# Kernel optimization log

Hardware: AMD Instinct MI355X
Metric: run time of the kernel (lower is better)

## Reference

```python
import jax, jax.numpy as jnp
import numpy as np

N_DYADIC = 0   # dyadic refinement order (init kwarg n)
SOLVER = 0     # first-order explicit finite-difference scheme (init kwarg solver)


def _solve_goursat(inc):
    """Solve Goursat PDE K_{p+1,q+1} = K_{p+1,q} + K_{p,q+1} - K_{p,q} + inc[p,q]*K_{p,q}
    with boundary K[0,:] = K[:,0] = 1. inc: [B, P, Q] -> returns K[P,Q] per pair: [B]."""
    B, P, Q = inc.shape
    dt = inc.dtype
    ones_b = jnp.ones((B,), dt)

    def row_step(prev_row, inc_row):
        # prev_row: [B, Q+1] = K[p, :]; inc_row: [B, Q]
        def col_step(k_left, t):
            k_diag, k_up, a = t  # K[p,q], K[p,q+1], inc[p,q], each [B]
            k_new = k_up + (k_left - k_diag) + a * k_diag
            return k_new, k_new
        xs = (prev_row[:, :-1].T, prev_row[:, 1:].T, inc_row.T)  # [Q, B] each
        _, tail = jax.lax.scan(col_step, ones_b, xs)              # tail: [Q, B]
        new_row = jnp.concatenate([ones_b[:, None], tail.T], axis=1)
        return new_row, None

    final_row, _ = jax.lax.scan(row_step, jnp.ones((B, Q + 1), dt), jnp.swapaxes(inc, 0, 1))
    return final_row[:, -1]


def _sig_kernel_gram(X, Y, n=N_DYADIC):
    """Signature-kernel Gram matrix. X: [A, M, D], Y: [B, N, D] -> [A, B]."""
    dX = X[:, 1:, :] - X[:, :-1, :]          # [A, M-1, D]
    dY = Y[:, 1:, :] - Y[:, :-1, :]          # [B, N-1, D]
    Minc = jnp.einsum('apd,bqd->abpq', dX, dY)  # pairwise increment inner products
    f = 2 ** n
    if f > 1:  # dyadic grid refinement: split each cell into f*f subcells
        Minc = jnp.repeat(jnp.repeat(Minc, f, axis=2), f, axis=3) / (f * f)
    A, B, P, Q = Minc.shape
    K = _solve_goursat(Minc.reshape(A * B, P, Q))
    return K.reshape(A, B)


def setup_inputs() -> dict:
    key = jax.random.key(0)
    kx, ky = jax.random.split(key)
    SCALE = 0.05  # small Brownian-like increments keep the exponential kernel tame
    X = jnp.cumsum(SCALE * jax.random.normal(kx, (64, 128, 64), dtype=jnp.float32), axis=1)
    Y = jnp.cumsum(SCALE * jax.random.normal(ky, (64, 128, 64), dtype=jnp.float32), axis=1)
    return {"X": X, "Y": Y}


def reference(X, Y):
    K_XX = _sig_kernel_gram(X, X)
    K_YY = _sig_kernel_gram(Y, Y)
    K_XY = _sig_kernel_gram(X, Y)
    dist = jnp.mean(K_XX) + jnp.mean(K_YY) - 2.0 * jnp.mean(K_XY)
    return jnp.mean((X[:, 0, :] - Y[:, 0, :]) ** 2) + dist
```

## Files before the change

### kernel.cpp

```cpp
#include <hip/hip_runtime.h>
#include <math.h>

#define DD 64
#define MM 128
#define RS 133
#define OD 66

typedef float  f32x4v __attribute__((ext_vector_type(4)));
typedef __bf16 bf16x8 __attribute__((ext_vector_type(8)));

#define FOR8(F) F(0) F(1) F(2) F(3) F(4) F(5) F(6) F(7)

union FragU { unsigned int u[4]; bf16x8 v; };

__device__ __forceinline__ unsigned cvtpk(float lo, float hi) {
    unsigned r;
    asm("v_cvt_pk_bf16_f32 %0, %1, %2" : "=v"(r) : "v"(lo), "v"(hi));
    return r;
}

__device__ __forceinline__ bf16x8 dfrag_hi(const float* __restrict__ r0,
                                           const float* __restrict__ r1) {
    float4 a0 = *(const float4*)r0, a1 = *(const float4*)(r0 + 4);
    float4 b0 = *(const float4*)r1, b1 = *(const float4*)(r1 + 4);
    FragU f;
    f.u[0] = cvtpk(b0.x - a0.x, b0.y - a0.y);
    f.u[1] = cvtpk(b0.z - a0.z, b0.w - a0.w);
    f.u[2] = cvtpk(b1.x - a1.x, b1.y - a1.y);
    f.u[3] = cvtpk(b1.z - a1.z, b1.w - a1.w);
    return f.v;
}

__device__ __forceinline__ void dfrag_hilo(const float* __restrict__ r0,
                                           const float* __restrict__ r1,
                                           bf16x8& hi, bf16x8& lo) {
    float4 a0 = *(const float4*)r0, a1 = *(const float4*)(r0 + 4);
    float4 b0 = *(const float4*)r1, b1 = *(const float4*)(r1 + 4);
    float d0 = b0.x - a0.x, d1 = b0.y - a0.y, d2 = b0.z - a0.z, d3 = b0.w - a0.w;
    float d4 = b1.x - a1.x, d5 = b1.y - a1.y, d6 = b1.z - a1.z, d7 = b1.w - a1.w;
    FragU H, L;
    H.u[0] = cvtpk(d0, d1); H.u[1] = cvtpk(d2, d3);
    H.u[2] = cvtpk(d4, d5); H.u[3] = cvtpk(d6, d7);
    float e0 = d0 - __uint_as_float(H.u[0] << 16);
    float e1 = d1 - __uint_as_float(H.u[0] & 0xffff0000u);
    float e2 = d2 - __uint_as_float(H.u[1] << 16);
    float e3 = d3 - __uint_as_float(H.u[1] & 0xffff0000u);
    float e4 = d4 - __uint_as_float(H.u[2] << 16);
    float e5 = d5 - __uint_as_float(H.u[2] & 0xffff0000u);
    float e6 = d6 - __uint_as_float(H.u[3] << 16);
    float e7 = d7 - __uint_as_float(H.u[3] & 0xffff0000u);
    L.u[0] = cvtpk(e0, e1); L.u[1] = cvtpk(e2, e3);
    L.u[2] = cvtpk(e4, e5); L.u[3] = cvtpk(e6, e7);
    hi = H.v; lo = L.v;
}

template<int CTRL, int RM, bool BC>
__device__ __forceinline__ float dpp_add(float x) {
    int t = __builtin_amdgcn_update_dpp(0, __float_as_int(x), CTRL, RM, 0xf, BC);
    return x + __int_as_float(t);
}
__device__ __forceinline__ float wave_incl_scan(float x) {
    x = dpp_add<0x111, 0xf, true >(x);
    x = dpp_add<0x112, 0xf, true >(x);
    x = dpp_add<0x114, 0xf, true >(x);
    x = dpp_add<0x118, 0xf, true >(x);
    x = dpp_add<0x142, 0xa, false>(x);
    x = dpp_add<0x143, 0xc, false>(x);
    return x;
}

__global__ __launch_bounds__(64, 3) void sig_goursat_kernel(
        const float* __restrict__ X, const float* __restrict__ Y,
        float* __restrict__ Kout)
{
    const int bid = blockIdx.x;
    int g, a, b;
    if (bid < 4160) {
        g = bid < 2080 ? 0 : 1;
        const int t = bid - g * 2080;
        float sq = sqrtf(4160.25f - 2.0f * (float)t);
        a = (int)(64.5f - sq);
        if (a < 0) a = 0; if (a > 63) a = 63;
        while (a > 0  && (a * (129 - a)) / 2 > t) --a;
        while (a < 63 && ((a + 1) * (128 - a)) / 2 <= t) ++a;
        b = a + (t - (a * (129 - a)) / 2);
    } else {
        const int t = bid - 4160;
        g = 2; a = t >> 6; b = t & 63;
    }

    const float* __restrict__ U = (g == 1 ? Y : X) + (size_t)a * (MM * DD);
    const float* __restrict__ V = (g == 0 ? X : Y) + (size_t)b * (MM * DD);

    const int lane = threadIdx.x;
    const int l15  = lane & 15;
    const int k8   = (lane >> 4) * 8;
    const int rowg = (lane >> 4) * 4;

    __shared__ float incL[16 * RS];

#define TBDECL(ct) bf16x8 tb0_##ct, tb1_##ct;
    FOR8(TBDECL)
#define TBUILD(ct) { int brow_ = ct * 16 + l15; if (brow_ > 126) brow_ = 126; \
        const float* vp_ = V + (size_t)brow_ * DD + k8; \
        tb0_##ct = dfrag_hi(vp_,      vp_ + DD); \
        tb1_##ct = dfrag_hi(vp_ + 32, vp_ + DD + 32); }
    FOR8(TBUILD)

    float KL0 = 1.0f, KL1 = 1.0f;
    const int wbase = rowg * RS + ((l15 & 1) ? OD : 0) + (l15 >> 1);

#define CTSTEP(ct) { f32x4v acc = {0.f, 0.f, 0.f, 0.f}; \
        acc = __builtin_amdgcn_mfma_f32_16x16x32_bf16(ahi0, tb0_##ct, acc, 0, 0, 0); \
        acc = __builtin_amdgcn_mfma_f32_16x16x32_bf16(alo0, tb0_##ct, acc, 0, 0, 0); \
        acc = __builtin_amdgcn_mfma_f32_16x16x32_bf16(ahi1, tb1_##ct, acc, 0, 0, 0); \
        acc = __builtin_amdgcn_mfma_f32_16x16x32_bf16(alo1, tb1_##ct, acc, 0, 0, 0); \
        const int w_ = wbase + ct * 8; \
        incL[w_]          = acc[0]; \
        incL[w_ + RS]     = acc[1]; \
        incL[w_ + 2*RS]   = acc[2]; \
        incL[w_ + 3*RS]   = acc[3]; }

#define SCANROW(r) { \
        const float iE = incL[(r) * RS + lane]; \
        const float iO = incL[(r) * RS + OD + lane]; \
        const float m0 = iE * KL0; \
        const float m1 = iO * KL1; \
        const float t_ = m0 + m1; \
        const float S_ = wave_incl_scan(t_); \
        const float ex = S_ - t_; \
        KL1 += ex + m0; \
        KL0 += ex; }

    for (int band = 0; band < 8; ++band) {
        int arow = band * 16 + l15; if (arow > 126) arow = 126;
        const float* ap = U + (size_t)arow * DD + k8;
        bf16x8 ahi0, alo0, ahi1, alo1;
        dfrag_hilo(ap,      ap + DD,      ahi0, alo0);
        dfrag_hilo(ap + 32, ap + DD + 32, ahi1, alo1);

        FOR8(CTSTEP)

        #pragma unroll
        for (int r = 0; r < 15; ++r) { SCANROW(r) }
        if (band < 7) { SCANROW(15) }
    }

    if (lane == 63) Kout[(size_t)g * 4096 + a * 64 + b] = KL1;
}

__global__ void sig_reduce_kernel(const float* __restrict__ X,
                                  const float* __restrict__ Y,
                                  const float* __restrict__ Kws,
                                  float* __restrict__ out)
{
    const int t = threadIdx.x;
    double accK = 0.0, acc2 = 0.0;
    for (int i = t; i < 4096; i += 256) {
        const int a = i >> 6, b = i & 63;
        if (a <= b) {
            const double w = (a == b) ? 1.0 : 2.0;
            accK += w * (double)Kws[i];
            accK += w * (double)Kws[4096 + i];
        }
        accK -= 2.0 * (double)Kws[8192 + i];
        const float df = X[(size_t)a * (MM * DD) + b] - Y[(size_t)a * (MM * DD) + b];
        acc2 += (double)df * (double)df;
    }
    __shared__ double red[256];
    red[t] = accK / 4096.0 + acc2 / 4096.0;
    __syncthreads();
    for (int s = 128; s > 0; s >>= 1) {
        if (t < s) red[t] += red[t + s];
        __syncthreads();
    }
    if (t == 0) out[0] = (float)red[0];
}

extern "C" void kernel_launch(void* const* d_in, const int* in_sizes, int n_in,
                              void* d_out, int out_size, void* d_ws, size_t ws_size,
                              hipStream_t stream) {
    const float* X = (const float*)d_in[0];
    const float* Y = (const float*)d_in[1];
    float* Kws = (float*)d_ws;
    float* out = (float*)d_out;

    sig_goursat_kernel<<<dim3(8256), dim3(64), 0, stream>>>(X, Y, Kws);
    sig_reduce_kernel<<<dim3(1), dim3(256), 0, stream>>>(X, Y, Kws, out);
}
```

Measured before the change: 140.1 us.

## Process two Goursat pairs per wave and drop bf16 lo-split for A operand

Each block now handles two row-paths against the same column path, so the V-side bf16 fragments are built once and reused for both. The two independent wave scans are interleaved, so each hides the other's DPP latency, and the grid size is halved. The A-operand hi/lo bf16 split is also dropped, which halves the MFMA count but lowers the precision of the increment inner products. Occupancy bound drops from 3 to 2 waves, and LDS use doubles.

```diff
diff --git a/kernel.cpp b/kernel.cpp
--- a/kernel.cpp
+++ b/kernel.cpp
@@ -5,6 +5,7 @@
 #define MM 128
 #define RS 133
 #define OD 66
+#define P1 2128
 
 typedef float  f32x4v __attribute__((ext_vector_type(4)));
 typedef __bf16 bf16x8 __attribute__((ext_vector_type(8)));
@@ -31,29 +32,6 @@
     return f.v;
 }
 
-__device__ __forceinline__ void dfrag_hilo(const float* __restrict__ r0,
-                                           const float* __restrict__ r1,
-                                           bf16x8& hi, bf16x8& lo) {
-    float4 a0 = *(const float4*)r0, a1 = *(const float4*)(r0 + 4);
-    float4 b0 = *(const float4*)r1, b1 = *(const float4*)(r1 + 4);
-    float d0 = b0.x - a0.x, d1 = b0.y - a0.y, d2 = b0.z - a0.z, d3 = b0.w - a0.w;
-    float d4 = b1.x - a1.x, d5 = b1.y - a1.y, d6 = b1.z - a1.z, d7 = b1.w - a1.w;
-    FragU H, L;
-    H.u[0] = cvtpk(d0, d1); H.u[1] = cvtpk(d2, d3);
-    H.u[2] = cvtpk(d4, d5); H.u[3] = cvtpk(d6, d7);
-    float e0 = d0 - __uint_as_float(H.u[0] << 16);
-    float e1 = d1 - __uint_as_float(H.u[0] & 0xffff0000u);
-    float e2 = d2 - __uint_as_float(H.u[1] << 16);
-    float e3 = d3 - __uint_as_float(H.u[1] & 0xffff0000u);
-    float e4 = d4 - __uint_as_float(H.u[2] << 16);
-    float e5 = d5 - __uint_as_float(H.u[2] & 0xffff0000u);
-    float e6 = d6 - __uint_as_float(H.u[3] << 16);
-    float e7 = d7 - __uint_as_float(H.u[3] & 0xffff0000u);
-    L.u[0] = cvtpk(e0, e1); L.u[1] = cvtpk(e2, e3);
-    L.u[2] = cvtpk(e4, e5); L.u[3] = cvtpk(e6, e7);
-    hi = H.v; lo = L.v;
-}
-
 template<int CTRL, int RM, bool BC>
 __device__ __forceinline__ float dpp_add(float x) {
     int t = __builtin_amdgcn_update_dpp(0, __float_as_int(x), CTRL, RM, 0xf, BC);
@@ -69,35 +47,40 @@
     return x;
 }
 
-__global__ __launch_bounds__(64, 3) void sig_goursat_kernel(
+__global__ __launch_bounds__(64, 2) void sig_goursat_kernel(
         const float* __restrict__ X, const float* __restrict__ Y,
         float* __restrict__ Kout)
 {
     const int bid = blockIdx.x;
-    int g, a, b;
-    if (bid < 4160) {
-        g = bid < 2080 ? 0 : 1;
-        const int t = bid - g * 2080;
-        float sq = sqrtf(4160.25f - 2.0f * (float)t);
-        a = (int)(64.5f - sq);
-        if (a < 0) a = 0; if (a > 63) a = 63;
-        while (a > 0  && (a * (129 - a)) / 2 > t) --a;
-        while (a < 63 && ((a + 1) * (128 - a)) / 2 <= t) ++a;
-        b = a + (t - (a * (129 - a)) / 2);
+    int g, a0, a1, bcol;
+    bool dup = false;
+    if (bid < 2112) {
+        g = bid < 1056 ? 0 : 1;
+        const int t = bid - g * 1056;
+        bcol = (int)(2.0f * sqrtf((float)t + 1.0f));
+        if (bcol > 63) bcol = 63;
+        while (bcol > 0  && ((bcol + 1) * (bcol + 1)) / 4 > t) --bcol;
+        while (bcol < 63 && ((bcol + 2) * (bcol + 2)) / 4 <= t) ++bcol;
+        const int j = t - ((bcol + 1) * (bcol + 1)) / 4;
+        a0 = 2 * j; a1 = 2 * j + 1;
+        if (a1 > bcol) { a1 = a0; dup = true; }
     } else {
-        const int t = bid - 4160;
-        g = 2; a = t >> 6; b = t & 63;
+        const int t = bid - 2112;
+        g = 2; bcol = t & 63;
+        a0 = (t >> 6) * 2; a1 = a0 + 1;
     }
 
-    const float* __restrict__ U = (g == 1 ? Y : X) + (size_t)a * (MM * DD);
-    const float* __restrict__ V = (g == 0 ? X : Y) + (size_t)b * (MM * DD);
+    const float* __restrict__ Ub = (g == 1 ? Y : X);
+    const float* __restrict__ U0 = Ub + (size_t)a0 * (MM * DD);
+    const float* __restrict__ U1 = Ub + (size_t)a1 * (MM * DD);
+    const float* __restrict__ V  = (g == 0 ? X : Y) + (size_t)bcol * (MM * DD);
 
     const int lane = threadIdx.x;
     const int l15  = lane & 15;
     const int k8   = (lane >> 4) * 8;
     const int rowg = (lane >> 4) * 4;
 
-    __shared__ float incL[16 * RS];
+    __shared__ float incL[2 * P1];
 
 #define TBDECL(ct) bf16x8 tb0_##ct, tb1_##ct;
     FOR8(TBDECL)
@@ -107,46 +90,65 @@
         tb1_##ct = dfrag_hi(vp_ + 32, vp_ + DD + 32); }
     FOR8(TBUILD)
 
-    float KL0 = 1.0f, KL1 = 1.0f;
+    float s0e = 1.0f, s0o = 1.0f;
+    float s1e = 1.0f, s1o = 1.0f;
     const int wbase = rowg * RS + ((l15 & 1) ? OD : 0) + (l15 >> 1);
 
-#define CTSTEP(ct) { f32x4v acc = {0.f, 0.f, 0.f, 0.f}; \
-        acc = __builtin_amdgcn_mfma_f32_16x16x32_bf16(ahi0, tb0_##ct, acc, 0, 0, 0); \
-        acc = __builtin_amdgcn_mfma_f32_16x16x32_bf16(alo0, tb0_##ct, acc, 0, 0, 0); \
-        acc = __builtin_amdgcn_mfma_f32_16x16x32_bf16(ahi1, tb1_##ct, acc, 0, 0, 0); \
-        acc = __builtin_amdgcn_mfma_f32_16x16x32_bf16(alo1, tb1_##ct, acc, 0, 0, 0); \
+#define CTSTEP2(ct) { \
+        f32x4v c0 = {0.f, 0.f, 0.f, 0.f}, c1 = {0.f, 0.f, 0.f, 0.f}; \
+        c0 = __builtin_amdgcn_mfma_f32_16x16x32_bf16(a0k0, tb0_##ct, c0, 0, 0, 0); \
+        c1 = __builtin_amdgcn_mfma_f32_16x16x32_bf16(a1k0, tb0_##ct, c1, 0, 0, 0); \
+        c0 = __builtin_amdgcn_mfma_f32_16x16x32_bf16(a0k1, tb1_##ct, c0, 0, 0, 0); \
+        c1 = __builtin_amdgcn_mfma_f32_16x16x32_bf16(a1k1, tb1_##ct, c1, 0, 0, 0); \
         const int w_ = wbase + ct * 8; \
-        incL[w_]          = acc[0]; \
-        incL[w_ + RS]     = acc[1]; \
-        incL[w_ + 2*RS]   = acc[2]; \
-        incL[w_ + 3*RS]   = acc[3]; }
+        incL[w_]             = c0[0]; \
+        incL[w_ + RS]        = c0[1]; \
+        incL[w_ + 2*RS]      = c0[2]; \
+        incL[w_ + 3*RS]      = c0[3]; \
+        incL[P1 + w_]        = c1[0]; \
+        incL[P1 + w_ + RS]   = c1[1]; \
+        incL[P1 + w_ + 2*RS] = c1[2]; \
+        incL[P1 + w_ + 3*RS] = c1[3]; }
 
-#define SCANROW(r) { \
-        const float iE = incL[(r) * RS + lane]; \
-        const float iO = incL[(r) * RS + OD + lane]; \
-        const float m0 = iE * KL0; \
-        const float m1 = iO * KL1; \
-        const float t_ = m0 + m1; \
-        const float S_ = wave_incl_scan(t_); \
-        const float ex = S_ - t_; \
-        KL1 += ex + m0; \
-        KL0 += ex; }
+#define SCANROW2(r) { \
+        const float iE0 = incL[(r) * RS + lane]; \
+        const float iO0 = incL[(r) * RS + OD + lane]; \
+        const float iE1 = incL[P1 + (r) * RS + lane]; \
+        const float iO1 = incL[P1 + (r) * RS + OD + lane]; \
+        const float m0a = iE0 * s0e; \
+        const float m1a = iO0 * s0o; \
+        const float m0b = iE1 * s1e; \
+        const float m1b = iO1 * s1o; \
+        const float ta  = m0a + m1a; \
+        const float tb  = m0b + m1b; \
+        const float Sa  = wave_incl_scan(ta); \
+        const float Sb  = wave_incl_scan(tb); \
+        const float exa = Sa - ta; \
+        const float exb = Sb - tb; \
+        s0o += exa + m0a;  s0e += exa; \
+        s1o += exb + m0b;  s1e += exb; }
 
     for (int band = 0; band < 8; ++band) {
         int arow = band * 16 + l15; if (arow > 126) arow = 126;
-        const float* ap = U + (size_t)arow * DD + k8;
-        bf16x8 ahi0, alo0, ahi1, alo1;
-        dfrag_hilo(ap,      ap + DD,      ahi0, alo0);
-        dfrag_hilo(ap + 32, ap + DD + 32, ahi1, alo1);
+        const float* ap0 = U0 + (size_t)arow * DD + k8;
+        const float* ap1 = U1 + (size_t)arow * DD + k8;
+        bf16x8 a0k0 = dfrag_hi(ap0,      ap0 + DD);
+        bf16x8 a0k1 = dfrag_hi(ap0 + 32, ap0 + DD + 32);
+        bf16x8 a1k0 = dfrag_hi(ap1,      ap1 + DD);
+        bf16x8 a1k1 = dfrag_hi(ap1 + 32, ap1 + DD + 32);
 
-        FOR8(CTSTEP)
+        FOR8(CTSTEP2)
 
         #pragma unroll
-        for (int r = 0; r < 15; ++r) { SCANROW(r) }
-        if (band < 7) { SCANROW(15) }
+        for (int r = 0; r < 15; ++r) { SCANROW2(r) }
+        if (band < 7) { SCANROW2(15) }
     }
 
-    if (lane == 63) Kout[(size_t)g * 4096 + a * 64 + b] = KL1;
+    if (lane == 63) {
+        float* kg = Kout + (size_t)g * 4096;
+        kg[a0 * 64 + bcol] = s0o;
+        if (!dup) kg[a1 * 64 + bcol] = s1o;
+    }
 }
 
 __global__ void sig_reduce_kernel(const float* __restrict__ X,
@@ -185,6 +187,6 @@
     float* Kws = (float*)d_ws;
     float* out = (float*)d_out;
 
-    sig_goursat_kernel<<<dim3(8256), dim3(64), 0, stream>>>(X, Y, Kws);
+    sig_goursat_kernel<<<dim3(4160), dim3(64), 0, stream>>>(X, Y, Kws);
     sig_reduce_kernel<<<dim3(1), dim3(256), 0, stream>>>(X, Y, Kws, out);
 }
```

New measurement: 125.4 us. -10.5%, faster.

## Split MFMA producer and scan consumer into separate waves with double buffering

Applied to the files above, without the earlier changes.

The kernel now uses two waves per block. One wave computes increment-matrix bands with MFMA into a double-buffered shared tile, and the other runs the wavefront scan on the previous band, with a __syncthreads per band. It also drops the bf16 hi/lo split-precision correction, halving MFMA work at some accuracy cost, and changes the LDS layout so the scan reads float2 pairs with prefetch. The aim is to overlap matrix compute with the serial scan. The producer/consumer barrier count must match exactly, and the accuracy loss from dropping the lo terms may matter.

```diff
diff --git a/kernel.cpp b/kernel.cpp
--- a/kernel.cpp
+++ b/kernel.cpp
@@ -3,8 +3,8 @@
 
 #define DD 64
 #define MM 128
-#define RS 133
-#define OD 66
+#define RSW 132
+#define BUFW 2112
 
 typedef float  f32x4v __attribute__((ext_vector_type(4)));
 typedef __bf16 bf16x8 __attribute__((ext_vector_type(8)));
@@ -31,29 +31,6 @@
     return f.v;
 }
 
-__device__ __forceinline__ void dfrag_hilo(const float* __restrict__ r0,
-                                           const float* __restrict__ r1,
-                                           bf16x8& hi, bf16x8& lo) {
-    float4 a0 = *(const float4*)r0, a1 = *(const float4*)(r0 + 4);
-    float4 b0 = *(const float4*)r1, b1 = *(const float4*)(r1 + 4);
-    float d0 = b0.x - a0.x, d1 = b0.y - a0.y, d2 = b0.z - a0.z, d3 = b0.w - a0.w;
-    float d4 = b1.x - a1.x, d5 = b1.y - a1.y, d6 = b1.z - a1.z, d7 = b1.w - a1.w;
-    FragU H, L;
-    H.u[0] = cvtpk(d0, d1); H.u[1] = cvtpk(d2, d3);
-    H.u[2] = cvtpk(d4, d5); H.u[3] = cvtpk(d6, d7);
-    float e0 = d0 - __uint_as_float(H.u[0] << 16);
-    float e1 = d1 - __uint_as_float(H.u[0] & 0xffff0000u);
-    float e2 = d2 - __uint_as_float(H.u[1] << 16);
-    float e3 = d3 - __uint_as_float(H.u[1] & 0xffff0000u);
-    float e4 = d4 - __uint_as_float(H.u[2] << 16);
-    float e5 = d5 - __uint_as_float(H.u[2] & 0xffff0000u);
-    float e6 = d6 - __uint_as_float(H.u[3] << 16);
-    float e7 = d7 - __uint_as_float(H.u[3] & 0xffff0000u);
-    L.u[0] = cvtpk(e0, e1); L.u[1] = cvtpk(e2, e3);
-    L.u[2] = cvtpk(e4, e5); L.u[3] = cvtpk(e6, e7);
-    hi = H.v; lo = L.v;
-}
-
 template<int CTRL, int RM, bool BC>
 __device__ __forceinline__ float dpp_add(float x) {
     int t = __builtin_amdgcn_update_dpp(0, __float_as_int(x), CTRL, RM, 0xf, BC);
@@ -69,7 +46,7 @@
     return x;
 }
 
-__global__ __launch_bounds__(64, 3) void sig_goursat_kernel(
+__global__ __launch_bounds__(128, 4) void sig_goursat_kernel(
         const float* __restrict__ X, const float* __restrict__ Y,
         float* __restrict__ Kout)
 {
@@ -89,64 +66,89 @@
         g = 2; a = t >> 6; b = t & 63;
     }
 
-    const float* __restrict__ U = (g == 1 ? Y : X) + (size_t)a * (MM * DD);
-    const float* __restrict__ V = (g == 0 ? X : Y) + (size_t)b * (MM * DD);
+    const int tid  = threadIdx.x;
+    const int wid  = tid >> 6;
+    const int lane = tid & 63;
 
-    const int lane = threadIdx.x;
-    const int l15  = lane & 15;
-    const int k8   = (lane >> 4) * 8;
-    const int rowg = (lane >> 4) * 4;
+    __shared__ float buf[2][BUFW];
 
-    __shared__ float incL[16 * RS];
+    if (wid == 0) {
+        const float* __restrict__ U = (g == 1 ? Y : X) + (size_t)a * (MM * DD);
+        const float* __restrict__ V = (g == 0 ? X : Y) + (size_t)b * (MM * DD);
+        const int l15  = lane & 15;
+        const int k8   = (lane >> 4) * 8;
+        const int rowg = (lane >> 4) * 4;
+        const int wbase = rowg * RSW + l15;
 
 #define TBDECL(ct) bf16x8 tb0_##ct, tb1_##ct;
-    FOR8(TBDECL)
+        FOR8(TBDECL)
 #define TBUILD(ct) { int brow_ = ct * 16 + l15; if (brow_ > 126) brow_ = 126; \
         const float* vp_ = V + (size_t)brow_ * DD + k8; \
         tb0_##ct = dfrag_hi(vp_,      vp_ + DD); \
         tb1_##ct = dfrag_hi(vp_ + 32, vp_ + DD + 32); }
-    FOR8(TBUILD)
+        FOR8(TBUILD)
 
-    float KL0 = 1.0f, KL1 = 1.0f;
-    const int wbase = rowg * RS + ((l15 & 1) ? OD : 0) + (l15 >> 1);
+#define CTSTEP(ct) { f32x4v c = {0.f, 0.f, 0.f, 0.f}; \
+        c = __builtin_amdgcn_mfma_f32_16x16x32_bf16(ak0, tb0_##ct, c, 0, 0, 0); \
+        c = __builtin_amdgcn_mfma_f32_16x16x32_bf16(ak1, tb1_##ct, c, 0, 0, 0); \
+        const int w_ = wbase + ct * 16; \
+        bp[w_]         = c[0]; \
+        bp[w_ + RSW]   = c[1]; \
+        bp[w_ + 2*RSW] = c[2]; \
+        bp[w_ + 3*RSW] = c[3]; }
 
-#define CTSTEP(ct) { f32x4v acc = {0.f, 0.f, 0.f, 0.f}; \
-        acc = __builtin_amdgcn_mfma_f32_16x16x32_bf16(ahi0, tb0_##ct, acc, 0, 0, 0); \
-        acc = __builtin_amdgcn_mfma_f32_16x16x32_bf16(alo0, tb0_##ct, acc, 0, 0, 0); \
-        acc = __builtin_amdgcn_mfma_f32_16x16x32_bf16(ahi1, tb1_##ct, acc, 0, 0, 0); \
-        acc = __builtin_amdgcn_mfma_f32_16x16x32_bf16(alo1, tb1_##ct, acc, 0, 0, 0); \
-        const int w_ = wbase + ct * 8; \
-        incL[w_]          = acc[0]; \
-        incL[w_ + RS]     = acc[1]; \
-        incL[w_ + 2*RS]   = acc[2]; \
-        incL[w_ + 3*RS]   = acc[3]; }
+        for (int band = 0; band < 8; ++band) {
+            int arow = band * 16 + l15; if (arow > 126) arow = 126;
+            const float* ap = U + (size_t)arow * DD + k8;
+            bf16x8 ak0 = dfrag_hi(ap,      ap + DD);
+            bf16x8 ak1 = dfrag_hi(ap + 32, ap + DD + 32);
+            float* bp = buf[band & 1];
+            FOR8(CTSTEP)
+            __syncthreads();
+        }
+    } else {
+        float KL0 = 1.0f, KL1 = 1.0f;
 
-#define SCANROW(r) { \
-        const float iE = incL[(r) * RS + lane]; \
-        const float iO = incL[(r) * RS + OD + lane]; \
-        const float m0 = iE * KL0; \
-        const float m1 = iO * KL1; \
+#define SCANROW1(e) { \
+        const float m0 = e.x * KL0; \
+        const float m1 = e.y * KL1; \
         const float t_ = m0 + m1; \
         const float S_ = wave_incl_scan(t_); \
         const float ex = S_ - t_; \
         KL1 += ex + m0; \
         KL0 += ex; }
 
-    for (int band = 0; band < 8; ++band) {
-        int arow = band * 16 + l15; if (arow > 126) arow = 126;
-        const float* ap = U + (size_t)arow * DD + k8;
-        bf16x8 ahi0, alo0, ahi1, alo1;
-        dfrag_hilo(ap,      ap + DD,      ahi0, alo0);
-        dfrag_hilo(ap + 32, ap + DD + 32, ahi1, alo1);
+        for (int band = 0; band < 7; ++band) {
+            __syncthreads();
+            const float2* pl = (const float2*)&buf[band & 1][2 * lane];
+            float2 e = pl[0];
+            float2 f = pl[66];
+            #pragma unroll
+            for (int r = 0; r < 14; ++r) {
+                float2 n = pl[(r + 2) * 66];
+                SCANROW1(e)
+                e = f; f = n;
+            }
+            SCANROW1(e)
+            SCANROW1(f)
+        }
+        {
+            __syncthreads();
+            const float2* pl = (const float2*)&buf[1][2 * lane];
+            float2 e = pl[0];
+            float2 f = pl[66];
+            #pragma unroll
+            for (int r = 0; r < 13; ++r) {
+                float2 n = pl[(r + 2) * 66];
+                SCANROW1(e)
+                e = f; f = n;
+            }
+            SCANROW1(e)
+            SCANROW1(f)
+        }
 
-        FOR8(CTSTEP)
-
-        #pragma unroll
-        for (int r = 0; r < 15; ++r) { SCANROW(r) }
-        if (band < 7) { SCANROW(15) }
+        if (lane == 63) Kout[(size_t)g * 4096 + a * 64 + b] = KL1;
     }
-
-    if (lane == 63) Kout[(size_t)g * 4096 + a * 64 + b] = KL1;
 }
 
 __global__ void sig_reduce_kernel(const float* __restrict__ X,
@@ -185,6 +187,6 @@
     float* Kws = (float*)d_ws;
     float* out = (float*)d_out;
 
-    sig_goursat_kernel<<<dim3(8256), dim3(64), 0, stream>>>(X, Y, Kws);
+    sig_goursat_kernel<<<dim3(8256), dim3(128), 0, stream>>>(X, Y, Kws);
     sig_reduce_kernel<<<dim3(1), dim3(256), 0, stream>>>(X, Y, Kws, out);
 }
```

After: 141.3 us. About the same (+0.8%).
